# Kernel optimization log

Measured on AMD Instinct MI355X. Metric: run time of the kernel, lower is better.

The kernel has to match this reference:

```python
import jax, jax.numpy as jnp
import numpy as np

B, T, I, H = 4, 128, 32, 64


def setup_inputs() -> dict:
    key = jax.random.key(0)
    k1, k2, k3 = jax.random.split(key, 3)
    x = jax.random.normal(k1, (B, T, I), dtype=jnp.float32)
    carry = jnp.zeros((B, H), dtype=jnp.float32)  # RNNCell.initialize_carry uses zeros
    # lecun_normal-like input kernel (default_kernel_init)
    Wi = jax.random.normal(k2, (I, H), dtype=jnp.float32) / np.float32(np.sqrt(I))
    # orthogonal recurrent kernel init
    Wh, _ = jnp.linalg.qr(jax.random.normal(k3, (H, H), dtype=jnp.float32))
    b = jnp.zeros((H,), dtype=jnp.float32)
    return {"carry": carry, "x": x, "Wi": Wi, "Wh": Wh, "b": b}


def reference(carry, x, Wi, Wh, b):
    # Vanilla RNN step: a = tanh(x_t @ Wi + h @ Wh + b), scanned over time (axis 1).
    # Per step we also emit the analytic forward-mode Jacobian of the new state
    # w.r.t. (Wi, Wh, b, carry) -- exactly what jacfwd(fn, argnums=(0,1)) computes.
    Hh = Wh.shape[0]
    Bb = carry.shape[0]
    eyeH = jnp.eye(Hh, dtype=x.dtype)
    eyeB = jnp.eye(Bb, dtype=x.dtype)

    def step(h, x_t):
        a = jnp.tanh(x_t @ Wi + h @ Wh + b)  # (B, H)
        g = 1.0 - a * a                      # tanh' at preactivation, (B, H)
        # d a[b,j] / d Wi[i,k] = g[b,j] * x[b,i] * delta(j,k)  -> (B, H, I, H)
        J_Wi = jnp.einsum('bj,bi,jk->bjik', g, x_t, eyeH)
        # d a[b,j] / d Wh[m,k] = g[b,j] * h[b,m] * delta(j,k)  -> (B, H, H, H)
        J_Wh = jnp.einsum('bj,bm,jk->bjmk', g, h, eyeH)
        # d a[b,j] / d b[k]    = g[b,j] * delta(j,k)           -> (B, H, H)
        J_b = jnp.einsum('bj,jk->bjk', g, eyeH)
        # d a[b,j] / d h[c,m]  = g[b,j] * Wh[m,j] * delta(b,c) -> (B, H, B, H)
        J_h = jnp.einsum('bj,mj,bc->bjcm', g, Wh, eyeB)
        return a, (a, J_Wi, J_Wh, J_b, J_h)

    final_carry, ys = jax.lax.scan(step, carry, jnp.moveaxis(x, 1, 0))
    # out_axes=1: time axis goes to position 1 of every output leaf
    out, J_Wi, J_Wh, J_b, J_h = jax.tree.map(lambda y: jnp.moveaxis(y, 0, 1), ys)
    return final_carry, out, J_Wi, J_Wh, J_b, J_h
```

## Files before the change

### kernel.cpp

```cpp
#include <hip/hip_runtime.h>
#include <math.h>

#define OFF_OUT   256u
#define OFF_JWI   33024u
#define OFF_JWH   67141888u
#define OFF_JB    201359616u
#define OFF_JH    203456768u

typedef float f32x4 __attribute__((ext_vector_type(4)));

static __device__ __forceinline__ float tanh_fast(float x) {
    float t = __expf(2.0f * x);
    return 1.0f - 2.0f / (t + 1.0f);
}

__global__ __launch_bounds__(256) void xwi_kernel(
    const float* __restrict__ x, const float* __restrict__ Wi,
    const float* __restrict__ bias, float* __restrict__ u)
{
    const int tid = threadIdx.x;
    const int row = blockIdx.x * 4 + (tid >> 6);
    const int j = tid & 63;
    const float* xr = x + row * 32;
    float acc = bias[j];
#pragma unroll
    for (int i = 0; i < 32; ++i) acc = fmaf(xr[i], Wi[i * 64 + j], acc);
    u[row * 64 + j] = acc;
}

__global__ __launch_bounds__(256) void scan_zero_kernel(
    const float* __restrict__ carry, const float* __restrict__ u,
    const float* __restrict__ Wh, float* __restrict__ out)
{
    const int tid = threadIdx.x;
    if (blockIdx.x == 0) {
        const int w = tid >> 6, j = tid & 63;
        float wcol[64];
#pragma unroll
        for (int m = 0; m < 64; ++m) wcol[m] = Wh[m * 64 + j];
        __shared__ __align__(16) float sh[256];
        sh[tid] = carry[tid];
        const float* ub = u + w * 8192;
        float* ob = out + OFF_OUT + w * 8192;
        const f32x4* shv = reinterpret_cast<const f32x4*>(sh + w * 64);
        float unext = ub[j];
        float a = 0.0f;
        for (int t = 0; t < 128; ++t) {
            const float pre = unext;
            if (t < 127) unext = ub[(t + 1) * 64 + j];
            float a0 = 0.f, a1 = 0.f, a2 = 0.f, a3 = 0.f;
#pragma unroll
            for (int mm = 0; mm < 16; ++mm) {
                const f32x4 hv = shv[mm];
                a0 = fmaf(hv.x, wcol[mm * 4 + 0], a0);
                a1 = fmaf(hv.y, wcol[mm * 4 + 1], a1);
                a2 = fmaf(hv.z, wcol[mm * 4 + 2], a2);
                a3 = fmaf(hv.w, wcol[mm * 4 + 3], a3);
            }
            a = tanh_fast(pre + (a0 + a1) + (a2 + a3));
            ob[t * 64 + j] = a;
            sh[tid] = a;
        }
        out[tid] = a;
    } else {
        const unsigned NW = (gridDim.x - 1u) * 4u;
        const unsigned l = tid & 63u;
        const f32x4 z = {0.f, 0.f, 0.f, 0.f};
        for (unsigned uu = (blockIdx.x - 1u) * 4u + (tid >> 6);
             uu < 425984u; uu += NW) {
            unsigned addr;
            if (uu < 131072u) {
                const unsigned r0 = uu * 8u;
                const unsigned j = (r0 >> 5) & 63u;
                addr = OFF_JWI + r0 * 64u + ((j < 32u) ? 32u : 0u)
                     + (l >> 3) * 64u + (l & 7u) * 4u;
            } else if (uu < 393216u) {
                const unsigned r0 = (uu - 131072u) * 8u;
                const unsigned j = (r0 >> 6) & 63u;
                addr = OFF_JWH + r0 * 64u + ((j < 32u) ? 32u : 0u)
                     + (l >> 3) * 64u + (l & 7u) * 4u;
            } else {
                addr = OFF_JH + (uu - 393216u) * 256u + l * 4u;
            }
            __builtin_nontemporal_store(z, reinterpret_cast<f32x4*>(out + addr));
        }
    }
}

__global__ __launch_bounds__(256) void diag_fill_kernel(
    const float* __restrict__ carry, const float* __restrict__ x,
    const float* __restrict__ Wh, float* __restrict__ out)
{
    const int tid = threadIdx.x;
    const unsigned NW = gridDim.x * 4u;
    const unsigned l = tid & 63u;
    const float* __restrict__ outh = out + OFF_OUT;

    for (unsigned uu = blockIdx.x * 4u + (tid >> 6); uu < 409600u; uu += NW) {
        unsigned addr;
        f32x4 r = {0.f, 0.f, 0.f, 0.f};
        if (uu < 131072u) {
            const unsigned r0 = uu * 8u;
            const unsigned bt = r0 >> 11;
            const unsigned j = (r0 >> 5) & 63u;
            const float a = outh[bt * 64u + j];
            const float g = 1.0f - a * a;
            const unsigned i = (r0 + (l >> 3)) & 31u;
            const float v = g * x[bt * 32u + i];
            const unsigned d = (j & 31u) - (l & 7u) * 4u;
            r.x = (d == 0u) ? v : 0.f; r.y = (d == 1u) ? v : 0.f;
            r.z = (d == 2u) ? v : 0.f; r.w = (d == 3u) ? v : 0.f;
            addr = OFF_JWI + r0 * 64u + ((j < 32u) ? 0u : 32u)
                 + (l >> 3) * 64u + (l & 7u) * 4u;
        } else if (uu < 393216u) {
            const unsigned r0 = (uu - 131072u) * 8u;
            const unsigned bt = r0 >> 12;
            const unsigned j = (r0 >> 6) & 63u;
            const unsigned t = bt & 127u, b = bt >> 7;
            const float a = outh[bt * 64u + j];
            const float g = 1.0f - a * a;
            const unsigned m = (r0 + (l >> 3)) & 63u;
            const float hv = (t == 0u) ? carry[b * 64u + m]
                                       : outh[(bt - 1u) * 64u + m];
            const float v = g * hv;
            const unsigned d = (j & 31u) - (l & 7u) * 4u;
            r.x = (d == 0u) ? v : 0.f; r.y = (d == 1u) ? v : 0.f;
            r.z = (d == 2u) ? v : 0.f; r.w = (d == 3u) ? v : 0.f;
            addr = OFF_JWH + r0 * 64u + ((j < 32u) ? 0u : 32u)
                 + (l >> 3) * 64u + (l & 7u) * 4u;
        } else if (uu < 401408u) {
            const unsigned p = (uu - 393216u) * 4u + (l >> 4);
            const unsigned j = p & 63u;
            const float a = outh[p];
            const float g = 1.0f - a * a;
            const unsigned d = j - (l & 15u) * 4u;
            r.x = (d == 0u) ? g : 0.f; r.y = (d == 1u) ? g : 0.f;
            r.z = (d == 2u) ? g : 0.f; r.w = (d == 3u) ? g : 0.f;
            addr = OFF_JB + p * 64u + (l & 15u) * 4u;
        } else {
            const unsigned p = (uu - 401408u) * 4u + (l >> 4);
            const unsigned bt = p >> 6, j = p & 63u, b = bt >> 7;
            const float a = outh[p];
            const float g = 1.0f - a * a;
            const unsigned k0 = (l & 15u) * 4u;
            r.x = g * Wh[(k0 + 0u) * 64u + j];
            r.y = g * Wh[(k0 + 1u) * 64u + j];
            r.z = g * Wh[(k0 + 2u) * 64u + j];
            r.w = g * Wh[(k0 + 3u) * 64u + j];
            addr = OFF_JH + p * 256u + b * 64u + k0;
        }
        __builtin_nontemporal_store(r, reinterpret_cast<f32x4*>(out + addr));
    }
}

extern "C" void kernel_launch(void* const* d_in, const int* in_sizes, int n_in,
                              void* d_out, int out_size, void* d_ws, size_t ws_size,
                              hipStream_t stream) {
    const float* carry = (const float*)d_in[0];
    const float* x     = (const float*)d_in[1];
    const float* Wi    = (const float*)d_in[2];
    const float* Wh    = (const float*)d_in[3];
    const float* bias  = (const float*)d_in[4];
    float* out = (float*)d_out;
    float* u = out + OFF_JB;

    xwi_kernel      <<<128, 256, 0, stream>>>(x, Wi, bias, u);
    scan_zero_kernel<<<2048, 256, 0, stream>>>(carry, u, Wh, out);
    diag_fill_kernel<<<2048, 256, 0, stream>>>(carry, x, Wh, out);
}
```

Before: 184.4 us.

## Zero Jacobian output linearly, then scatter only diagonal-bearing vectors

The zero-fill blocks now clear the whole Jacobian region with a plain linear, fully coalesced stream of vector stores, replacing the earlier strided off-diagonal-half pattern. The fill kernel then rewrites only the 16-byte chunks that hold diagonal entries for J_Wi, J_Wh and J_b, plus the dense J_h rows, so it issues far fewer stores. The x@Wi result is staged in the output's `out` slice and overwritten in place by the scan, instead of living in the J_b region. The trade-off is somewhat more total bytes written, since diagonal chunks are written twice, and sparse scattered 16-byte stores in the second kernel.

```diff
diff --git a/kernel.cpp b/kernel.cpp
--- a/kernel.cpp
+++ b/kernel.cpp
@@ -6,6 +6,7 @@
 #define OFF_JWH   67141888u
 #define OFF_JB    201359616u
 #define OFF_JH    203456768u
+#define OUT_TOTAL 211845376u
 
 typedef float f32x4 __attribute__((ext_vector_type(4)));
 
@@ -16,7 +17,7 @@
 
 __global__ __launch_bounds__(256) void xwi_kernel(
     const float* __restrict__ x, const float* __restrict__ Wi,
-    const float* __restrict__ bias, float* __restrict__ u)
+    const float* __restrict__ bias, float* __restrict__ out)
 {
     const int tid = threadIdx.x;
     const int row = blockIdx.x * 4 + (tid >> 6);
@@ -25,12 +26,12 @@
     float acc = bias[j];
 #pragma unroll
     for (int i = 0; i < 32; ++i) acc = fmaf(xr[i], Wi[i * 64 + j], acc);
-    u[row * 64 + j] = acc;
+    out[OFF_OUT + row * 64 + j] = acc;
 }
 
 __global__ __launch_bounds__(256) void scan_zero_kernel(
-    const float* __restrict__ carry, const float* __restrict__ u,
-    const float* __restrict__ Wh, float* __restrict__ out)
+    const float* __restrict__ carry, const float* __restrict__ Wh,
+    float* __restrict__ out)
 {
     const int tid = threadIdx.x;
     if (blockIdx.x == 0) {
@@ -40,8 +41,7 @@
         for (int m = 0; m < 64; ++m) wcol[m] = Wh[m * 64 + j];
         __shared__ __align__(16) float sh[256];
         sh[tid] = carry[tid];
-        const float* ub = u + w * 8192;
-        float* ob = out + OFF_OUT + w * 8192;
+        float* ub = out + OFF_OUT + w * 8192;
         const f32x4* shv = reinterpret_cast<const f32x4*>(sh + w * 64);
         float unext = ub[j];
         float a = 0.0f;
@@ -58,32 +58,19 @@
                 a3 = fmaf(hv.w, wcol[mm * 4 + 3], a3);
             }
             a = tanh_fast(pre + (a0 + a1) + (a2 + a3));
-            ob[t * 64 + j] = a;
+            ub[t * 64 + j] = a;
             sh[tid] = a;
         }
         out[tid] = a;
     } else {
-        const unsigned NW = (gridDim.x - 1u) * 4u;
-        const unsigned l = tid & 63u;
+        const unsigned startv = OFF_JWI >> 2;
+        const unsigned endv   = OUT_TOTAL >> 2;
+        const unsigned stride = (gridDim.x - 1u) * 256u;
         const f32x4 z = {0.f, 0.f, 0.f, 0.f};
-        for (unsigned uu = (blockIdx.x - 1u) * 4u + (tid >> 6);
-             uu < 425984u; uu += NW) {
-            unsigned addr;
-            if (uu < 131072u) {
-                const unsigned r0 = uu * 8u;
-                const unsigned j = (r0 >> 5) & 63u;
-                addr = OFF_JWI + r0 * 64u + ((j < 32u) ? 32u : 0u)
-                     + (l >> 3) * 64u + (l & 7u) * 4u;
-            } else if (uu < 393216u) {
-                const unsigned r0 = (uu - 131072u) * 8u;
-                const unsigned j = (r0 >> 6) & 63u;
-                addr = OFF_JWH + r0 * 64u + ((j < 32u) ? 32u : 0u)
-                     + (l >> 3) * 64u + (l & 7u) * 4u;
-            } else {
-                addr = OFF_JH + (uu - 393216u) * 256u + l * 4u;
-            }
-            __builtin_nontemporal_store(z, reinterpret_cast<f32x4*>(out + addr));
-        }
+        f32x4* o4 = reinterpret_cast<f32x4*>(out);
+        for (unsigned v = startv + (blockIdx.x - 1u) * 256u + tid;
+             v < endv; v += stride)
+            __builtin_nontemporal_store(z, o4 + v);
     }
 }
 
@@ -92,62 +79,56 @@
     const float* __restrict__ Wh, float* __restrict__ out)
 {
     const int tid = threadIdx.x;
-    const unsigned NW = gridDim.x * 4u;
+    const unsigned nW = gridDim.x * 4u;
     const unsigned l = tid & 63u;
     const float* __restrict__ outh = out + OFF_OUT;
 
-    for (unsigned uu = blockIdx.x * 4u + (tid >> 6); uu < 409600u; uu += NW) {
+    for (unsigned w = blockIdx.x * 4u + (tid >> 6); w < 57856u; w += nW) {
         unsigned addr;
-        f32x4 r = {0.f, 0.f, 0.f, 0.f};
-        if (uu < 131072u) {
-            const unsigned r0 = uu * 8u;
-            const unsigned bt = r0 >> 11;
-            const unsigned j = (r0 >> 5) & 63u;
-            const float a = outh[bt * 64u + j];
-            const float g = 1.0f - a * a;
-            const unsigned i = (r0 + (l >> 3)) & 31u;
-            const float v = g * x[bt * 32u + i];
-            const unsigned d = (j & 31u) - (l & 7u) * 4u;
-            r.x = (d == 0u) ? v : 0.f; r.y = (d == 1u) ? v : 0.f;
-            r.z = (d == 2u) ? v : 0.f; r.w = (d == 3u) ? v : 0.f;
-            addr = OFF_JWI + r0 * 64u + ((j < 32u) ? 0u : 32u)
-                 + (l >> 3) * 64u + (l & 7u) * 4u;
-        } else if (uu < 393216u) {
-            const unsigned r0 = (uu - 131072u) * 8u;
-            const unsigned bt = r0 >> 12;
-            const unsigned j = (r0 >> 6) & 63u;
+        f32x4 r;
+        if (w < 32768u) {
+            const unsigned bt = w >> 6, j = w & 63u;
             const unsigned t = bt & 127u, b = bt >> 7;
             const float a = outh[bt * 64u + j];
             const float g = 1.0f - a * a;
-            const unsigned m = (r0 + (l >> 3)) & 63u;
-            const float hv = (t == 0u) ? carry[b * 64u + m]
-                                       : outh[(bt - 1u) * 64u + m];
+            const float hv = (t == 0u) ? carry[b * 64u + l]
+                                       : outh[(bt - 1u) * 64u + l];
             const float v = g * hv;
-            const unsigned d = (j & 31u) - (l & 7u) * 4u;
+            const unsigned d = j & 3u;
             r.x = (d == 0u) ? v : 0.f; r.y = (d == 1u) ? v : 0.f;
             r.z = (d == 2u) ? v : 0.f; r.w = (d == 3u) ? v : 0.f;
-            addr = OFF_JWH + r0 * 64u + ((j < 32u) ? 0u : 32u)
-                 + (l >> 3) * 64u + (l & 7u) * 4u;
-        } else if (uu < 401408u) {
-            const unsigned p = (uu - 393216u) * 4u + (l >> 4);
+            addr = OFF_JWH + w * 4096u + l * 64u + (j & ~3u);
+        } else if (w < 49152u) {
+            const unsigned pair = (w - 32768u) * 2u + (l >> 5);
+            const unsigned bt = pair >> 6, j = pair & 63u;
+            const float a = outh[bt * 64u + j];
+            const float g = 1.0f - a * a;
+            const unsigned i = l & 31u;
+            const float v = g * x[bt * 32u + i];
+            const unsigned d = j & 3u;
+            r.x = (d == 0u) ? v : 0.f; r.y = (d == 1u) ? v : 0.f;
+            r.z = (d == 2u) ? v : 0.f; r.w = (d == 3u) ? v : 0.f;
+            addr = OFF_JWI + (pair * 32u + i) * 64u + (j & ~3u);
+        } else if (w < 49664u) {
+            const unsigned p = (w - 49152u) * 64u + l;
             const unsigned j = p & 63u;
             const float a = outh[p];
             const float g = 1.0f - a * a;
-            const unsigned d = j - (l & 15u) * 4u;
+            const unsigned d = j & 3u;
             r.x = (d == 0u) ? g : 0.f; r.y = (d == 1u) ? g : 0.f;
             r.z = (d == 2u) ? g : 0.f; r.w = (d == 3u) ? g : 0.f;
-            addr = OFF_JB + p * 64u + (l & 15u) * 4u;
+            addr = OFF_JB + p * 64u + (j & ~3u);
         } else {
-            const unsigned p = (uu - 401408u) * 4u + (l >> 4);
+            const unsigned p = (w - 49664u) * 4u + (l >> 4);
             const unsigned bt = p >> 6, j = p & 63u, b = bt >> 7;
             const float a = outh[p];
             const float g = 1.0f - a * a;
-            const unsigned k0 = (l & 15u) * 4u;
-            r.x = g * Wh[(k0 + 0u) * 64u + j];
-            r.y = g * Wh[(k0 + 1u) * 64u + j];
-            r.z = g * Wh[(k0 + 2u) * 64u + j];
-            r.w = g * Wh[(k0 + 3u) * 64u + j];
-            addr = OFF_JH + p * 256u + b * 64u + k0;
+            const unsigned m0 = (l & 15u) * 4u;
+            r.x = g * Wh[(m0 + 0u) * 64u + j];
+            r.y = g * Wh[(m0 + 1u) * 64u + j];
+            r.z = g * Wh[(m0 + 2u) * 64u + j];
+            r.w = g * Wh[(m0 + 3u) * 64u + j];
+            addr = OFF_JH + p * 256u + b * 64u + m0;
         }
         __builtin_nontemporal_store(r, reinterpret_cast<f32x4*>(out + addr));
     }
@@ -162,9 +143,8 @@
     const float* Wh    = (const float*)d_in[3];
     const float* bias  = (const float*)d_in[4];
     float* out = (float*)d_out;
-    float* u = out + OFF_JB;
 
-    xwi_kernel      <<<128, 256, 0, stream>>>(x, Wi, bias, u);
-    scan_zero_kernel<<<2048, 256, 0, stream>>>(carry, u, Wh, out);
+    xwi_kernel      <<<128, 256, 0, stream>>>(x, Wi, bias, out);
+    scan_zero_kernel<<<2048, 256, 0, stream>>>(carry, Wh, out);
     diag_fill_kernel<<<2048, 256, 0, stream>>>(carry, x, Wh, out);
 }
```

Result: slower. 320.8 us (+73.9%).
